# Kernel optimization log

Measured on AMD Instinct MI355X. Metric: run time of the kernel, lower is better.

The kernel has to match this reference:

```python
import jax, jax.numpy as jnp
import numpy as np

NH = 12          # num attention heads
EPS = 1e-6       # layer-norm eps
B, T_, S_, H, E, IE = 8, 8, 196, 768, 4, 768  # IE = intermediate_size // num_experts


def layernorm(x, g, b):
    m = jnp.mean(x, axis=-1, keepdims=True)
    v = jnp.var(x, axis=-1, keepdims=True)
    return (x - m) / jnp.sqrt(v + EPS) * g + b


def mha(x, qkv_w, qkv_b, proj_w, proj_b):
    # x: [B', N, H]
    Bp, N, Hh = x.shape
    hd = Hh // NH
    qkv = (x @ qkv_w + qkv_b).reshape(Bp, N, 3, NH, hd).transpose(2, 0, 3, 1, 4)
    q, k, v = qkv[0], qkv[1], qkv[2]                      # [B', nh, N, hd]
    attn = jax.nn.softmax(jnp.einsum('bhqd,bhkd->bhqk', q, k) * (hd ** -0.5), axis=-1)
    out = jnp.einsum('bhqk,bhkd->bhqd', attn, v).transpose(0, 2, 1, 3).reshape(Bp, N, Hh)
    return out @ proj_w + proj_b


def moe_mlp(x, gate_up, down, eids):
    # x: [B, N, H]; gate_up: [E, H, 2*IE]; down: [E, IE, H]; eids: [N]
    sel = jax.nn.one_hot(eids, gate_up.shape[0], dtype=x.dtype)  # [N, E]
    gu = jnp.einsum('bnh,ehk,ne->bnk', x, gate_up, sel)          # per-token expert gate+up
    gate, up = gu[..., :IE], gu[..., IE:]
    inter = jax.nn.silu(gate) * up                               # SwiGLU
    return jnp.einsum('bni,eih,ne->bnh', inter, down, sel)


def setup_inputs() -> dict:
    key = jax.random.key(0)
    ks = jax.random.split(key, 16)
    w = lambda k, shp: (jax.random.normal(k, shp, dtype=jnp.float32) * 0.02)
    inp = {
        'x': jax.random.normal(ks[0], (B, T_ * S_, H), dtype=jnp.float32),
        'qkv_w_s': w(ks[1], (H, 3 * H)), 'qkv_b_s': jnp.zeros((3 * H,), jnp.float32),
        'proj_w_s': w(ks[2], (H, H)),    'proj_b_s': jnp.zeros((H,), jnp.float32),
        'qkv_w_t': w(ks[3], (H, 3 * H)), 'qkv_b_t': jnp.zeros((3 * H,), jnp.float32),
        'proj_w_t': w(ks[4], (H, H)),    'proj_b_t': jnp.zeros((H,), jnp.float32),
        'ln_s_g': jnp.ones((H,), jnp.float32), 'ln_s_b': jnp.zeros((H,), jnp.float32),
        'ln_t_g': jnp.ones((H,), jnp.float32), 'ln_t_b': jnp.zeros((H,), jnp.float32),
        'ln_m_g': jnp.ones((H,), jnp.float32), 'ln_m_b': jnp.zeros((H,), jnp.float32),
        'gate_up_proj': w(ks[5], (E, H, 2 * IE)),
        'down_proj': w(ks[6], (E, IE, H)),
        'T': T_, 'S': S_,
        'expert_ids': jax.random.randint(ks[7], (T_ * S_,), 0, E, dtype=jnp.int32),
    }
    return inp


def reference(x, qkv_w_s, qkv_b_s, proj_w_s, proj_b_s,
              qkv_w_t, qkv_b_t, proj_w_t, proj_b_t,
              ln_s_g, ln_s_b, ln_t_g, ln_t_b, ln_m_g, ln_m_b,
              gate_up_proj, down_proj, T, S, expert_ids):
    Bb, N, Hh = x.shape
    # 1) spatial attention over S patches within each of B*T frames
    xs = layernorm(x, ln_s_g, ln_s_b).reshape(Bb * T, S, Hh)
    xs = mha(xs, qkv_w_s, qkv_b_s, proj_w_s, proj_b_s).reshape(Bb, T * S, Hh)
    x = x + xs
    # 2) temporal attention over T frames at each of B*S spatial positions
    xt = layernorm(x, ln_t_g, ln_t_b).reshape(Bb, T, S, Hh).transpose(0, 2, 1, 3).reshape(Bb * S, T, Hh)
    xt = mha(xt, qkv_w_t, qkv_b_t, proj_w_t, proj_b_t)
    xt = xt.reshape(Bb, S, T, Hh).transpose(0, 2, 1, 3).reshape(Bb, T * S, Hh)
    x = x + xt
    # 3) token-routed MoE MLP
    x = x + moe_mlp(layernorm(x, ln_m_g, ln_m_b), gate_up_proj, down_proj, expert_ids)
    return x
```

## Files before the change

### kernel.cpp

```cpp
#include <hip/hip_runtime.h>

typedef __bf16 bf16;
typedef bf16 bf16x8 __attribute__((ext_vector_type(8)));
typedef float f32x4 __attribute__((ext_vector_type(4)));

#define BB 8
#define TT 8
#define SS 196
#define NTOK 1568
#define ROWS 12544
#define HH 768
#define HD 64

__device__ __forceinline__ void gload16(const void* g, void* l) {
  __builtin_amdgcn_global_load_lds(
      (const __attribute__((address_space(1))) void*)g,
      (__attribute__((address_space(3))) void*)l, 16, 0, 0);
}

__global__ __launch_bounds__(256)
void transpose_w(const float* __restrict__ in, bf16* __restrict__ out, int K, int N) {
  in  += (size_t)blockIdx.z * K * N;
  out += (size_t)blockIdx.z * K * N;
  __shared__ float tile[64][65];
  const int k0 = blockIdx.x * 64, n0 = blockIdx.y * 64;
  const int tx = threadIdx.x & 63, ty = threadIdx.x >> 6;
  #pragma unroll
  for (int rr = ty; rr < 64; rr += 4)
    tile[rr][tx] = in[(size_t)(k0 + rr) * N + n0 + tx];
  __syncthreads();
  #pragma unroll
  for (int rr = ty; rr < 64; rr += 4)
    out[(size_t)(n0 + rr) * K + k0 + tx] = (bf16)tile[tx][rr];
}

__global__ __launch_bounds__(256)
void transpose_gu(const float* __restrict__ in, bf16* __restrict__ out) {
  const int K = 768, N = 1536;
  in  += (size_t)blockIdx.z * K * N;
  out += (size_t)blockIdx.z * K * N;
  __shared__ float tile[64][65];
  const int k0 = blockIdx.x * 64, n0 = blockIdx.y * 64;
  const int tx = threadIdx.x & 63, ty = threadIdx.x >> 6;
  const int s = n0 >> 6;
  #pragma unroll
  for (int rr = ty; rr < 64; rr += 4) {
    const int src = (tx < 32) ? (s * 32 + tx) : (768 + s * 32 + tx - 32);
    tile[rr][tx] = in[(size_t)(k0 + rr) * N + src];
  }
  __syncthreads();
  #pragma unroll
  for (int rr = ty; rr < 64; rr += 4)
    out[(size_t)(n0 + rr) * K + k0 + tx] = (bf16)tile[tx][rr];
}

template<typename TI>
__global__ __launch_bounds__(256)
void ln_kernel(const TI* __restrict__ x, const float* __restrict__ g,
               const float* __restrict__ b, bf16* __restrict__ out) {
  const int row = blockIdx.x * 4 + (threadIdx.x >> 6);
  const int lane = threadIdx.x & 63;
  const TI* xr = x + (size_t)row * HH;
  float v[12];
  float sum = 0.f, sq = 0.f;
  #pragma unroll
  for (int i = 0; i < 12; ++i) {
    v[i] = (float)xr[lane + i * 64];
    sum += v[i];
    sq += v[i] * v[i];
  }
  #pragma unroll
  for (int off = 32; off > 0; off >>= 1) {
    sum += __shfl_xor(sum, off);
    sq  += __shfl_xor(sq, off);
  }
  const float mean = sum * (1.f / 768.f);
  const float var = sq * (1.f / 768.f) - mean * mean;
  const float inv = rsqrtf(var + 1e-6f);
  bf16* op = out + (size_t)row * HH;
  #pragma unroll
  for (int i = 0; i < 12; ++i) {
    const int c = lane + i * 64;
    op[c] = (bf16)((v[i] - mean) * inv * g[c] + b[c]);
  }
}

template<bool MOE, bool BIAS, bool RESID, bool RB16, bool OBF16, bool GUFUSE>
__global__ __launch_bounds__(256, 2)
void gemmDP(const bf16* __restrict__ A, const bf16* __restrict__ BT,
            const float* __restrict__ bias, const void* __restrict__ resid,
            float* __restrict__ outF, bf16* __restrict__ outB,
            int N, int K, int NMT,
            const int* __restrict__ perm, const int4* __restrict__ descs,
            const int* __restrict__ meta) {
  __shared__ __align__(16) bf16 lds[3 * 12288];
  __shared__ int rowLds[128];

  const int tid = threadIdx.x;
  const int G = gridDim.x;
  int work;
  {
    const int q = G >> 3, r = G & 7, xcd = blockIdx.x & 7, pos = blockIdx.x >> 3;
    work = (xcd < r ? xcd * (q + 1) : r * (q + 1) + (xcd - r) * q) + pos;
  }
  int M0 = 0, N0, ncnt = 16;
  if constexpr (MOE) {
    const int ntile = work % NMT, desc = work / NMT;
    if (desc >= meta[0]) return;
    int4 d = descs[desc];
    BT += (size_t)d.x * N * K;
    ncnt = d.z;
    N0 = ntile * 256;
    if (tid < 128) {
      const int nl = tid >> 3, b = tid & 7;
      const int n = perm[d.y + (nl < ncnt ? nl : ncnt - 1)];
      rowLds[tid] = b * NTOK + n;
    }
    __syncthreads();
  } else {
    const int mt = work / NMT, nt = work % NMT;
    M0 = mt * 128;
    N0 = nt * 256;
  }

  const int w = tid >> 6, lane = tid & 63;
  const int wr = w >> 1, wc = w & 1;
  const int lr = lane & 15, lg = lane >> 4;

  const int r0 = tid >> 2;
  const int sseg = ((tid & 3) ^ ((tid >> 3) & 3)) * 8;
  int arow0, arow1;
  if constexpr (MOE) {
    arow0 = rowLds[r0];
    arow1 = rowLds[64 + r0];
  } else {
    arow0 = M0 + r0;
    arow1 = M0 + 64 + r0;
  }
  const bf16* aP0 = A + (size_t)arow0 * K + sseg;
  const bf16* aP1 = A + (size_t)arow1 * K + sseg;
  const bf16* bP0 = BT + (size_t)(N0 + r0) * K + sseg;
  const bf16* bP1 = BT + (size_t)(N0 + 64 + r0) * K + sseg;
  const bf16* bP2 = BT + (size_t)(N0 + 128 + r0) * K + sseg;
  const bf16* bP3 = BT + (size_t)(N0 + 192 + r0) * K + sseg;

  auto STG = [&](int kt) {
    bf16* buf = lds + (kt % 3) * 12288;
    const int ko = kt << 5;
    gload16(aP0 + ko, buf + tid * 8);
    gload16(aP1 + ko, buf + 2048 + tid * 8);
    gload16(bP0 + ko, buf + 4096 + tid * 8);
    gload16(bP1 + ko, buf + 6144 + tid * 8);
    gload16(bP2 + ko, buf + 8192 + tid * 8);
    gload16(bP3 + ko, buf + 10240 + tid * 8);
  };

  const int axr = (lg ^ ((lr >> 1) & 3)) * 8;

  f32x4 acc[4][8] = {};
  const int NT = K >> 5;

  STG(0); STG(1);

  for (int t = 0; t < NT; ++t) {
    if (t + 1 < NT) { asm volatile("s_waitcnt vmcnt(6)" ::: "memory"); }
    else            { asm volatile("s_waitcnt vmcnt(0)" ::: "memory"); }
    __builtin_amdgcn_s_barrier();
    asm volatile("" ::: "memory");

    const bf16* Ab = lds + (t % 3) * 12288;
    const bf16* Bb = Ab + 4096;
    bf16x8 a[4], b[8];
    #pragma unroll
    for (int mf = 0; mf < 4; ++mf) {
      const int row = wr * 64 + mf * 16 + lr;
      a[mf] = *(const bf16x8*)(Ab + row * 32 + axr);
    }
    #pragma unroll
    for (int nf = 0; nf < 8; ++nf) {
      const int row = wc * 128 + nf * 16 + lr;
      b[nf] = *(const bf16x8*)(Bb + row * 32 + axr);
    }
    if (t + 2 < NT) STG(t + 2);

    asm volatile("s_waitcnt lgkmcnt(0)" ::: "memory");
    __builtin_amdgcn_sched_barrier(0);
    __builtin_amdgcn_s_setprio(1);
    #pragma unroll
    for (int mf = 0; mf < 4; ++mf)
      #pragma unroll
      for (int nf = 0; nf < 8; ++nf)
        acc[mf][nf] = __builtin_amdgcn_mfma_f32_16x16x32_bf16(a[mf], b[nf], acc[mf][nf], 0, 0, 0);
    __builtin_amdgcn_s_setprio(0);
    asm volatile("" ::: "memory");
  }

  #pragma unroll
  for (int m = 0; m < 4; ++m) {
    #pragma unroll
    for (int j = 0; j < 4; ++j) {
      const int r = wr * 64 + m * 16 + lg * 4 + j;
      if (MOE && ((r >> 3) >= ncnt)) continue;
      const size_t grow = MOE ? (size_t)rowLds[r] : (size_t)(M0 + r);
      if constexpr (GUFUSE) {
        const size_t rbase = grow * 768;
        #pragma unroll
        for (int n = 0; n < 8; ++n) {
          if ((n & 3) >= 2) continue;
          const int icol = (N0 >> 1) + (wc * 2 + (n >> 2)) * 32 + (n & 3) * 16 + lr;
          const float g = acc[m][n][j], u = acc[m][n + 2][j];
          outB[rbase + icol] = (bf16)(g / (1.f + __expf(-g)) * u);
        }
      } else {
        const size_t rbase = grow * N;
        #pragma unroll
        for (int n = 0; n < 8; ++n) {
          const int gcol = N0 + wc * 128 + n * 16 + lr;
          float v = acc[m][n][j];
          if constexpr (BIAS)  v += bias[gcol];
          if constexpr (RESID) {
            if constexpr (RB16) v += (float)((const bf16*)resid)[rbase + gcol];
            else                v += ((const float*)resid)[rbase + gcol];
          }
          if constexpr (OBF16) outB[rbase + gcol] = (bf16)v;
          else                 outF[rbase + gcol] = v;
        }
      }
    }
  }
}

#define SPAD 208
#define VST 232
__global__ __launch_bounds__(512)
void attn_spatial(const bf16* __restrict__ qkv, bf16* __restrict__ out) {
  __shared__ __align__(16) bf16 Ks[SPAD * 64];
  __shared__ __align__(16) bf16 Vt[64 * VST];
  __shared__ __align__(16) bf16 Pb[8][16 * VST];

  const int bp = blockIdx.x, h = blockIdx.y;
  const int tid = threadIdx.x;
  const int w = tid >> 6, lane = tid & 63;
  const int lr = lane & 15, lg = lane >> 4;
  const size_t base = (size_t)bp * SS * 2304 + h * HD;

  for (int cb = w * 64; cb < SPAD * 8; cb += 512) {
    const int c = cb + lane;
    const int row = c >> 3, seg = c & 7;
    const int srow = row < SS ? row : SS - 1;
    const int sseg = seg ^ (row & 7);
    gload16(qkv + base + (size_t)srow * 2304 + 768 + sseg * 8, Ks + cb * 8);
  }
  for (int t = tid; t < 224 * 8; t += 512) {
    const int k = t >> 3, dseg = t & 7;
    const int sk = k < SS ? k : SS - 1;
    bf16x8 v = *(const bf16x8*)(qkv + base + (size_t)sk * 2304 + 1536 + dseg * 8);
    #pragma unroll
    for (int i = 0; i < 8; ++i) Vt[(dseg * 8 + i) * VST + k] = v[i];
  }
  bf16* Pw = Pb[w];
  for (int i = lane; i < 256; i += 64)
    Pw[(i >> 4) * VST + 208 + (i & 15)] = (bf16)0.f;
  __syncthreads();

  for (int t = w; t < 13; t += 8) {
    const int q0 = t * 16;
    const int qr = q0 + lr;
    const bf16* qp = qkv + base + (size_t)(qr < SS ? qr : SS - 1) * 2304 + lg * 8;
    const bf16x8 af0 = *(const bf16x8*)qp;
    const bf16x8 af1 = *(const bf16x8*)(qp + 32);

    f32x4 sc[13];
    #pragma unroll
    for (int f = 0; f < 13; ++f) sc[f] = (f32x4){0.f, 0.f, 0.f, 0.f};
    #pragma unroll
    for (int f = 0; f < 13; ++f) {
      const int key = f * 16 + lr;
      const bf16x8 bv0 = *(const bf16x8*)&Ks[key * 64 + ((lg) ^ (key & 7)) * 8];
      const bf16x8 bv1 = *(const bf16x8*)&Ks[key * 64 + ((4 + lg) ^ (key & 7)) * 8];
      sc[f] = __builtin_amdgcn_mfma_f32_16x16x32_bf16(af0, bv0, sc[f], 0, 0, 0);
      sc[f] = __builtin_amdgcn_mfma_f32_16x16x32_bf16(af1, bv1, sc[f], 0, 0, 0);
    }
    #pragma unroll
    for (int f = 0; f < 13; ++f)
      #pragma unroll
      for (int j = 0; j < 4; ++j) sc[f][j] *= 0.125f;
    if (192 + lr >= SS)
      #pragma unroll
      for (int j = 0; j < 4; ++j) sc[12][j] = -1e30f;

    float mx[4], ls[4];
    #pragma unroll
    for (int j = 0; j < 4; ++j) {
      float m = sc[0][j];
      #pragma unroll
      for (int f = 1; f < 13; ++f) m = fmaxf(m, sc[f][j]);
      #pragma unroll
      for (int off = 1; off < 16; off <<= 1) m = fmaxf(m, __shfl_xor(m, off));
      mx[j] = m;
    }
    #pragma unroll
    for (int j = 0; j < 4; ++j) ls[j] = 0.f;
    #pragma unroll
    for (int f = 0; f < 13; ++f) {
      #pragma unroll
      for (int j = 0; j < 4; ++j) {
        const float p = __expf(sc[f][j] - mx[j]);
        ls[j] += p;
        Pw[(lg * 4 + j) * VST + f * 16 + lr] = (bf16)p;
      }
    }
    #pragma unroll
    for (int j = 0; j < 4; ++j) {
      #pragma unroll
      for (int off = 1; off < 16; off <<= 1) ls[j] += __shfl_xor(ls[j], off);
      ls[j] = 1.f / ls[j];
    }

    f32x4 oacc[4];
    #pragma unroll
    for (int n = 0; n < 4; ++n) oacc[n] = (f32x4){0.f, 0.f, 0.f, 0.f};
    #pragma unroll
    for (int kb = 0; kb < 7; ++kb) {
      const bf16x8 pa = *(const bf16x8*)&Pw[lr * VST + kb * 32 + lg * 8];
      #pragma unroll
      for (int n = 0; n < 4; ++n) {
        const bf16x8 bv = *(const bf16x8*)&Vt[(n * 16 + lr) * VST + kb * 32 + lg * 8];
        oacc[n] = __builtin_amdgcn_mfma_f32_16x16x32_bf16(pa, bv, oacc[n], 0, 0, 0);
      }
    }
    #pragma unroll
    for (int j = 0; j < 4; ++j) {
      const int row = q0 + lg * 4 + j;
      if (row < SS) {
        bf16* op = out + ((size_t)bp * SS + row) * 768 + h * HD;
        #pragma unroll
        for (int n = 0; n < 4; ++n) op[n * 16 + lr] = (bf16)(oacc[n][j] * ls[j]);
      }
    }
  }
}

__global__ __launch_bounds__(256)
void attn_temporal(const bf16* __restrict__ qkv, bf16* __restrict__ out) {
  const int pair = blockIdx.x * 4 + (threadIdx.x >> 6);
  const int lane = threadIdx.x & 63;
  const int h = pair % 12;
  const int bs = pair / 12;
  const int b = bs / SS, s = bs - b * SS;
  const size_t row0 = (size_t)b * NTOK + s;
  const int q = lane >> 3, k = lane & 7;
  const bf16* qr = qkv + (row0 + (size_t)q * SS) * 2304 + h * HD;
  const bf16* kr = qkv + (row0 + (size_t)k * SS) * 2304 + 768 + h * HD;
  float sc = 0.f;
  #pragma unroll
  for (int j = 0; j < 8; ++j) {
    bf16x8 qv = ((const bf16x8*)qr)[j];
    bf16x8 kv = ((const bf16x8*)kr)[j];
    #pragma unroll
    for (int d = 0; d < 8; ++d) sc += (float)qv[d] * (float)kv[d];
  }
  sc *= 0.125f;
  float mxv = sc;
  #pragma unroll
  for (int off = 1; off < 8; off <<= 1) mxv = fmaxf(mxv, __shfl_xor(mxv, off));
  float p = __expf(sc - mxv);
  float sum = p;
  #pragma unroll
  for (int off = 1; off < 8; off <<= 1) sum += __shfl_xor(sum, off);
  p /= sum;

  const int dg = lane & 7;
  float o[8] = {0, 0, 0, 0, 0, 0, 0, 0};
  #pragma unroll
  for (int kk = 0; kk < 8; ++kk) {
    const float pk = __shfl(p, (lane & 56) + kk);
    const bf16* vr = qkv + (row0 + (size_t)kk * SS) * 2304 + 1536 + h * HD + dg * 8;
    bf16x8 vv = *(const bf16x8*)vr;
    #pragma unroll
    for (int j = 0; j < 8; ++j) o[j] += pk * (float)vv[j];
  }
  bf16* op = out + (row0 + (size_t)q * SS) * 768 + h * HD + dg * 8;
  bf16x8 ov;
  #pragma unroll
  for (int j = 0; j < 8; ++j) ov[j] = (bf16)o[j];
  *(bf16x8*)op = ov;
}

__global__ __launch_bounds__(256)
void sort_moe(const int* __restrict__ eids, int* __restrict__ perm,
              int4* __restrict__ descs, int* __restrict__ meta) {
  __shared__ int cnt[4], base[4], cur[4];
  const int tid = threadIdx.x;
  if (tid < 4) cnt[tid] = 0;
  __syncthreads();
  for (int n = tid; n < NTOK; n += 256) atomicAdd(&cnt[eids[n]], 1);
  __syncthreads();
  if (tid == 0) {
    int off = 0;
    for (int e = 0; e < 4; ++e) { base[e] = off; cur[e] = off; off += cnt[e]; }
  }
  __syncthreads();
  for (int n = tid; n < NTOK; n += 256) {
    const int pos = atomicAdd(&cur[eids[n]], 1);
    perm[pos] = n;
  }
  if (tid == 0) {
    int t = 0;
    for (int e = 0; e < 4; ++e)
      for (int st = 0; st < cnt[e]; st += 16) {
        const int c = cnt[e] - st;
        descs[t++] = make_int4(e, base[e] + st, c < 16 ? c : 16, 0);
      }
    meta[0] = t;
  }
}

extern "C" void kernel_launch(void* const* d_in, const int* in_sizes, int n_in,
                              void* d_out, int out_size, void* d_ws, size_t ws_size,
                              hipStream_t stream) {
  (void)in_sizes; (void)n_in; (void)out_size; (void)ws_size;
  const float* x        = (const float*)d_in[0];
  const float* qkv_w_s  = (const float*)d_in[1];
  const float* qkv_b_s  = (const float*)d_in[2];
  const float* proj_w_s = (const float*)d_in[3];
  const float* proj_b_s = (const float*)d_in[4];
  const float* qkv_w_t  = (const float*)d_in[5];
  const float* qkv_b_t  = (const float*)d_in[6];
  const float* proj_w_t = (const float*)d_in[7];
  const float* proj_b_t = (const float*)d_in[8];
  const float* ln_s_g   = (const float*)d_in[9];
  const float* ln_s_b   = (const float*)d_in[10];
  const float* ln_t_g   = (const float*)d_in[11];
  const float* ln_t_b   = (const float*)d_in[12];
  const float* ln_m_g   = (const float*)d_in[13];
  const float* ln_m_b   = (const float*)d_in[14];
  const float* gate_up  = (const float*)d_in[15];
  const float* down_w   = (const float*)d_in[16];
  const int* expert_ids = (const int*)d_in[19];
  float* out = (float*)d_out;

  char* ws = (char*)d_ws;
  bf16* qkvsT   = (bf16*)(ws + 0);
  bf16* projsT  = (bf16*)(ws + 3538944);
  bf16* qkvtT   = (bf16*)(ws + 4718592);
  bf16* projtT  = (bf16*)(ws + 8257536);
  bf16* guT     = (bf16*)(ws + 9437184);
  bf16* downT   = (bf16*)(ws + 18874368);
  bf16* lnbuf   = (bf16*)(ws + 23592960);
  bf16* qkvbuf  = (bf16*)(ws + 42860544);
  bf16* attnbuf = (bf16*)(ws + 100663296);
  bf16* x1b     = (bf16*)(ws + 119930880);
  int*  perm    = (int*)(ws + 158466048);
  int4* descs   = (int4*)(ws + 158472320);
  int*  meta    = (int*)(ws + 158473952);

  const dim3 blk(256);
  const dim3 blk512(512);

  transpose_w<<<dim3(12, 36, 1), blk, 0, stream>>>(qkv_w_s, qkvsT, 768, 2304);
  transpose_w<<<dim3(12, 12, 1), blk, 0, stream>>>(proj_w_s, projsT, 768, 768);
  transpose_w<<<dim3(12, 36, 1), blk, 0, stream>>>(qkv_w_t, qkvtT, 768, 2304);
  transpose_w<<<dim3(12, 12, 1), blk, 0, stream>>>(proj_w_t, projtT, 768, 768);
  transpose_gu<<<dim3(12, 24, 4), blk, 0, stream>>>(gate_up, guT);
  transpose_w<<<dim3(12, 12, 4), blk, 0, stream>>>(down_w, downT, 768, 768);

  ln_kernel<float><<<3136, blk, 0, stream>>>(x, ln_s_g, ln_s_b, lnbuf);
  gemmDP<false, true, false, false, true, false><<<dim3(98 * 9), blk, 0, stream>>>(
      lnbuf, qkvsT, qkv_b_s, nullptr, nullptr, qkvbuf, 2304, 768, 9,
      nullptr, nullptr, nullptr);
  attn_spatial<<<dim3(64, 12), blk512, 0, stream>>>(qkvbuf, attnbuf);
  gemmDP<false, true, true, false, true, false><<<dim3(98 * 3), blk, 0, stream>>>(
      attnbuf, projsT, proj_b_s, x, nullptr, x1b, 768, 768, 3,
      nullptr, nullptr, nullptr);

  ln_kernel<bf16><<<3136, blk, 0, stream>>>(x1b, ln_t_g, ln_t_b, lnbuf);
  gemmDP<false, true, false, false, true, false><<<dim3(98 * 9), blk, 0, stream>>>(
      lnbuf, qkvtT, qkv_b_t, nullptr, nullptr, qkvbuf, 2304, 768, 9,
      nullptr, nullptr, nullptr);
  attn_temporal<<<4704, blk, 0, stream>>>(qkvbuf, attnbuf);
  gemmDP<false, true, true, true, false, false><<<dim3(98 * 3), blk, 0, stream>>>(
      attnbuf, projtT, proj_b_t, x1b, out, nullptr, 768, 768, 3,
      nullptr, nullptr, nullptr);

  ln_kernel<float><<<3136, blk, 0, stream>>>(out, ln_m_g, ln_m_b, lnbuf);
  sort_moe<<<1, blk, 0, stream>>>(expert_ids, perm, descs, meta);
  gemmDP<true, false, false, false, true, true><<<dim3(6 * 102), blk, 0, stream>>>(
      lnbuf, guT, nullptr, nullptr, nullptr, qkvbuf, 1536, 768, 6,
      perm, descs, meta);
  gemmDP<true, false, true, false, false, false><<<dim3(3 * 102), blk, 0, stream>>>(
      qkvbuf, downT, nullptr, out, out, nullptr, 768, 768, 3,
      perm, descs, meta);
}
```

Baseline: 391.7 us.

## Write MoE layernorm output in expert-sorted order to make GEMM A-loads contiguous

The sort kernel now also emits an inverse permutation, and the MoE layernorm writes each row directly to its expert-sorted position (token-major, batch-minor). The gate/up GEMM then reads A rows contiguously from M0 = d.y*8 instead of gathering through rowLds, and writes its intermediate in the same sorted layout. Only the down-projection keeps the scatter through rowLds to place results back into the residual output. This removes the gathered, scattered row accesses in the first MoE GEMM at the cost of a scattered store in the layernorm. It also reuses the attention buffer region for the inverse permutation, which relies on that buffer being dead by then.

```diff
diff --git a/kernel.cpp b/kernel.cpp
--- a/kernel.cpp
+++ b/kernel.cpp
@@ -85,7 +85,40 @@
   }
 }
 
-template<bool MOE, bool BIAS, bool RESID, bool RB16, bool OBF16, bool GUFUSE>
+__global__ __launch_bounds__(256)
+void ln_moe_kernel(const float* __restrict__ x, const float* __restrict__ g,
+                   const float* __restrict__ b, const int* __restrict__ invp,
+                   bf16* __restrict__ out) {
+  const int row = blockIdx.x * 4 + (threadIdx.x >> 6);
+  const int lane = threadIdx.x & 63;
+  const float* xr = x + (size_t)row * HH;
+  float v[12];
+  float sum = 0.f, sq = 0.f;
+  #pragma unroll
+  for (int i = 0; i < 12; ++i) {
+    v[i] = xr[lane + i * 64];
+    sum += v[i];
+    sq += v[i] * v[i];
+  }
+  #pragma unroll
+  for (int off = 32; off > 0; off >>= 1) {
+    sum += __shfl_xor(sum, off);
+    sq  += __shfl_xor(sq, off);
+  }
+  const float mean = sum * (1.f / 768.f);
+  const float var = sq * (1.f / 768.f) - mean * mean;
+  const float inv = rsqrtf(var + 1e-6f);
+  const int bb = row / NTOK, n = row - bb * NTOK;
+  bf16* op = out + ((size_t)invp[n] * 8 + bb) * HH;
+  #pragma unroll
+  for (int i = 0; i < 12; ++i) {
+    const int c = lane + i * 64;
+    op[c] = (bf16)((v[i] - mean) * inv * g[c] + b[c]);
+  }
+}
+
+template<bool MOE, bool BIAS, bool RESID, bool RB16, bool OBF16, bool GUFUSE,
+         bool SCATTER>
 __global__ __launch_bounds__(256, 2)
 void gemmDP(const bf16* __restrict__ A, const bf16* __restrict__ BT,
             const float* __restrict__ bias, const void* __restrict__ resid,
@@ -111,12 +144,15 @@
     BT += (size_t)d.x * N * K;
     ncnt = d.z;
     N0 = ntile * 256;
-    if (tid < 128) {
-      const int nl = tid >> 3, b = tid & 7;
-      const int n = perm[d.y + (nl < ncnt ? nl : ncnt - 1)];
-      rowLds[tid] = b * NTOK + n;
-    }
-    __syncthreads();
+    M0 = d.y * 8;
+    if constexpr (SCATTER) {
+      if (tid < 128) {
+        const int nl = tid >> 3, b = tid & 7;
+        const int n = perm[d.y + (nl < ncnt ? nl : ncnt - 1)];
+        rowLds[tid] = b * NTOK + n;
+      }
+      __syncthreads();
+    }
   } else {
     const int mt = work / NMT, nt = work % NMT;
     M0 = mt * 128;
@@ -129,13 +165,10 @@
 
   const int r0 = tid >> 2;
   const int sseg = ((tid & 3) ^ ((tid >> 3) & 3)) * 8;
-  int arow0, arow1;
+  int arow0 = M0 + r0, arow1 = M0 + 64 + r0;
   if constexpr (MOE) {
-    arow0 = rowLds[r0];
-    arow1 = rowLds[64 + r0];
-  } else {
-    arow0 = M0 + r0;
-    arow1 = M0 + 64 + r0;
+    arow0 = arow0 < ROWS ? arow0 : ROWS - 1;
+    arow1 = arow1 < ROWS ? arow1 : ROWS - 1;
   }
   const bf16* aP0 = A + (size_t)arow0 * K + sseg;
   const bf16* aP1 = A + (size_t)arow1 * K + sseg;
@@ -201,7 +234,9 @@
     for (int j = 0; j < 4; ++j) {
       const int r = wr * 64 + m * 16 + lg * 4 + j;
       if (MOE && ((r >> 3) >= ncnt)) continue;
-      const size_t grow = MOE ? (size_t)rowLds[r] : (size_t)(M0 + r);
+      size_t grow;
+      if constexpr (MOE && SCATTER) grow = (size_t)rowLds[r];
+      else                          grow = (size_t)(M0 + r);
       if constexpr (GUFUSE) {
         const size_t rbase = grow * 768;
         #pragma unroll
@@ -389,7 +424,8 @@
 
 __global__ __launch_bounds__(256)
 void sort_moe(const int* __restrict__ eids, int* __restrict__ perm,
-              int4* __restrict__ descs, int* __restrict__ meta) {
+              int* __restrict__ invp, int4* __restrict__ descs,
+              int* __restrict__ meta) {
   __shared__ int cnt[4], base[4], cur[4];
   const int tid = threadIdx.x;
   if (tid < 4) cnt[tid] = 0;
@@ -404,6 +440,7 @@
   for (int n = tid; n < NTOK; n += 256) {
     const int pos = atomicAdd(&cur[eids[n]], 1);
     perm[pos] = n;
+    invp[n] = pos;
   }
   if (tid == 0) {
     int t = 0;
@@ -454,6 +491,7 @@
   int*  perm    = (int*)(ws + 158466048);
   int4* descs   = (int4*)(ws + 158472320);
   int*  meta    = (int*)(ws + 158473952);
+  int*  invp    = (int*)(ws + 100663296);
 
   const dim3 blk(256);
   const dim3 blk512(512);
@@ -466,29 +504,29 @@
   transpose_w<<<dim3(12, 12, 4), blk, 0, stream>>>(down_w, downT, 768, 768);
 
   ln_kernel<float><<<3136, blk, 0, stream>>>(x, ln_s_g, ln_s_b, lnbuf);
-  gemmDP<false, true, false, false, true, false><<<dim3(98 * 9), blk, 0, stream>>>(
+  gemmDP<false, true, false, false, true, false, false><<<dim3(98 * 9), blk, 0, stream>>>(
       lnbuf, qkvsT, qkv_b_s, nullptr, nullptr, qkvbuf, 2304, 768, 9,
       nullptr, nullptr, nullptr);
   attn_spatial<<<dim3(64, 12), blk512, 0, stream>>>(qkvbuf, attnbuf);
-  gemmDP<false, true, true, false, true, false><<<dim3(98 * 3), blk, 0, stream>>>(
+  gemmDP<false, true, true, false, true, false, false><<<dim3(98 * 3), blk, 0, stream>>>(
       attnbuf, projsT, proj_b_s, x, nullptr, x1b, 768, 768, 3,
       nullptr, nullptr, nullptr);
 
   ln_kernel<bf16><<<3136, blk, 0, stream>>>(x1b, ln_t_g, ln_t_b, lnbuf);
-  gemmDP<false, true, false, false, true, false><<<dim3(98 * 9), blk, 0, stream>>>(
+  gemmDP<false, true, false, false, true, false, false><<<dim3(98 * 9), blk, 0, stream>>>(
       lnbuf, qkvtT, qkv_b_t, nullptr, nullptr, qkvbuf, 2304, 768, 9,
       nullptr, nullptr, nullptr);
   attn_temporal<<<4704, blk, 0, stream>>>(qkvbuf, attnbuf);
-  gemmDP<false, true, true, true, false, false><<<dim3(98 * 3), blk, 0, stream>>>(
+  gemmDP<false, true, true, true, false, false, false><<<dim3(98 * 3), blk, 0, stream>>>(
       attnbuf, projtT, proj_b_t, x1b, out, nullptr, 768, 768, 3,
       nullptr, nullptr, nullptr);
 
-  ln_kernel<float><<<3136, blk, 0, stream>>>(out, ln_m_g, ln_m_b, lnbuf);
-  sort_moe<<<1, blk, 0, stream>>>(expert_ids, perm, descs, meta);
-  gemmDP<true, false, false, false, true, true><<<dim3(6 * 102), blk, 0, stream>>>(
+  sort_moe<<<1, blk, 0, stream>>>(expert_ids, perm, invp, descs, meta);
+  ln_moe_kernel<<<3136, blk, 0, stream>>>(out, ln_m_g, ln_m_b, invp, lnbuf);
+  gemmDP<true, false, false, false, true, true, false><<<dim3(6 * 102), blk, 0, stream>>>(
       lnbuf, guT, nullptr, nullptr, nullptr, qkvbuf, 1536, 768, 6,
       perm, descs, meta);
-  gemmDP<true, false, true, false, false, false><<<dim3(3 * 102), blk, 0, stream>>>(
+  gemmDP<true, false, true, false, false, false, true><<<dim3(3 * 102), blk, 0, stream>>>(
       qkvbuf, downT, nullptr, out, out, nullptr, 768, 768, 3,
       perm, descs, meta);
 }
```

Result: no change. 387.0 us (-1.2%).
